# Performance work log

Measured on AMD Instinct MI355X. Metric: run time of the kernel, lower is better.

Reference implementation:

```python
import jax, jax.numpy as jnp
import numpy as np

N_NODES = 100000
N_EDGES = 1600000
IN_DIM, HID_DIM, OUT_DIM = 128, 128, 47
BN_EPS = 1e-5


def setup_inputs() -> dict:
    key = jax.random.key(0)
    ks = jax.random.split(key, 12)
    x = jax.random.normal(ks[0], (N_NODES, IN_DIM), dtype=jnp.float32)
    edge_index = jax.random.randint(ks[1], (2, N_EDGES), 0, N_NODES, dtype=jnp.int32)
    def glorot(k, fan_in, fan_out):
        s = jnp.sqrt(6.0 / (fan_in + fan_out))
        return jax.random.uniform(k, (fan_in, fan_out), jnp.float32, -s, s)
    return {
        "x": x,
        "edge_index": edge_index,
        "W0": glorot(ks[2], IN_DIM, HID_DIM), "b0": jnp.zeros((HID_DIM,), jnp.float32),
        "W1": glorot(ks[3], HID_DIM, HID_DIM), "b1": jnp.zeros((HID_DIM,), jnp.float32),
        "W2": glorot(ks[4], HID_DIM, OUT_DIM), "b2": jnp.zeros((OUT_DIM,), jnp.float32),
        "g0": jnp.ones((HID_DIM,), jnp.float32), "be0": jnp.zeros((HID_DIM,), jnp.float32),
        "g1": jnp.ones((HID_DIM,), jnp.float32), "be1": jnp.zeros((HID_DIM,), jnp.float32),
    }


def _gcn_norm(edge_index, n_nodes):
    # add self-loops, compute sym-normalized edge weights (PyG GCNConv default)
    loop = jnp.arange(n_nodes, dtype=edge_index.dtype)
    src = jnp.concatenate([edge_index[0], loop])
    dst = jnp.concatenate([edge_index[1], loop])
    deg = jax.ops.segment_sum(jnp.ones_like(dst, dtype=jnp.float32), dst,
                              num_segments=n_nodes)
    dinv = jnp.where(deg > 0, jax.lax.rsqrt(deg), 0.0)
    norm = dinv[src] * dinv[dst]  # [E + N]
    return src, dst, norm


def _conv(x, W, b, src, dst, norm, n_nodes):
    h = x @ W                                   # [N, d_out]
    msg = h[src] * norm[:, None]                # gather + scale
    out = jax.ops.segment_sum(msg, dst, num_segments=n_nodes)
    return out + b


def _batchnorm(h, gamma, beta):
    mean = jnp.mean(h, axis=0)
    var = jnp.mean(jnp.square(h - mean), axis=0)  # biased var (torch BN)
    return (h - mean) * jax.lax.rsqrt(var + BN_EPS) * gamma + beta


def reference(x, edge_index, W0, b0, W1, b1, W2, b2, g0, be0, g1, be1):
    n = x.shape[0]
    src, dst, norm = _gcn_norm(edge_index, n)
    h = _conv(x, W0, b0, src, dst, norm, n)
    h = jax.nn.relu(_batchnorm(h, g0, be0))     # dropout = identity (eval)
    h = _conv(h, W1, b1, src, dst, norm, n)
    h = jax.nn.relu(_batchnorm(h, g1, be1))
    h = _conv(h, W2, b2, src, dst, norm, n)
    return jax.nn.log_softmax(h, axis=-1)
```

## Files before the change

kernel.cpp:

```cpp
#include <hip/hip_runtime.h>
#include <math.h>

#define N_NODES 100000
#define N_EDGES 1600000
#define HID 128
#define OUTD 47
#define OSTR 48

#define NPB 128
#define NB 782
#define BCAP 2560
#define CHUNK 2048
#define NCHB 782
#define CWB 64

typedef short bf16x8 __attribute__((ext_vector_type(8)));
typedef float f32x4 __attribute__((ext_vector_type(4)));

__device__ inline unsigned short f2bf(float x) {
    union { float f; unsigned int u; } v; v.f = x;
    unsigned int r = v.u + 0x7fffu + ((v.u >> 16) & 1u);
    return (unsigned short)(r >> 16);
}
__device__ inline float bf_lo(unsigned int u) { return __uint_as_float(u << 16); }
__device__ inline float bf_hi(unsigned int u) { return __uint_as_float(u & 0xffff0000u); }

__device__ inline unsigned int src_chunk(unsigned int s) {
    return (s * 42950u) >> 28;
}


__global__ __launch_bounds__(256) void binA_k(
    const int* __restrict__ src, const int* __restrict__ dst,
    int* __restrict__ gcur, unsigned int* __restrict__ binned,
    const float* __restrict__ W0, const float* __restrict__ W1, const float* __restrict__ W2,
    unsigned short* __restrict__ Wt0, unsigned short* __restrict__ Wt1,
    unsigned short* __restrict__ Wt2)
{
    __shared__ unsigned int sortedL[CHUNK];
    __shared__ unsigned short bucketOf[CHUNK];
    __shared__ int cntL[NB];
    __shared__ int excL[NB];
    __shared__ int curL[NB];
    __shared__ int gposL[NB];
    __shared__ int partial[256];

    int t = threadIdx.x;

    if (blockIdx.x >= NCHB) {
        int i = (blockIdx.x - NCHB) * 256 + t;
        if (i < 16384) {
            int n = i >> 7, k = i & 127;
            Wt0[i] = f2bf(W0[k * 128 + n]);
            Wt1[i] = f2bf(W1[k * 128 + n]);
        }
        if (i < 48 * 128) {
            int n = i >> 7, k = i & 127;
            Wt2[i] = (n < OUTD) ? f2bf(W2[k * OUTD + n]) : (unsigned short)0;
        }
        return;
    }

    int e0 = blockIdx.x * CHUNK;

    for (int i = t; i < NB; i += 256) cntL[i] = 0;
    __syncthreads();

    for (int i = t; i < CHUNK; i += 256) {
        int e = e0 + i;
        if (e < N_EDGES) atomicAdd(&cntL[dst[e] >> 7], 1);
    }
    __syncthreads();

    int b4 = t * 4;
    int c0 = (b4 + 0 < NB) ? cntL[b4 + 0] : 0;
    int c1 = (b4 + 1 < NB) ? cntL[b4 + 1] : 0;
    int c2 = (b4 + 2 < NB) ? cntL[b4 + 2] : 0;
    int c3 = (b4 + 3 < NB) ? cntL[b4 + 3] : 0;
    int lsum = c0 + c1 + c2 + c3;
    partial[t] = lsum;
    __syncthreads();
    for (int off = 1; off < 256; off <<= 1) {
        int x = (t >= off) ? partial[t - off] : 0;
        __syncthreads();
        partial[t] += x;
        __syncthreads();
    }
    int pbase = partial[t] - lsum;
    if (b4 + 0 < NB) { excL[b4 + 0] = pbase;                curL[b4 + 0] = pbase; }
    if (b4 + 1 < NB) { excL[b4 + 1] = pbase + c0;           curL[b4 + 1] = pbase + c0; }
    if (b4 + 2 < NB) { excL[b4 + 2] = pbase + c0 + c1;      curL[b4 + 2] = pbase + c0 + c1; }
    if (b4 + 3 < NB) { excL[b4 + 3] = pbase + c0 + c1 + c2; curL[b4 + 3] = pbase + c0 + c1 + c2; }
    __syncthreads();

    int tot = partial[255];

    for (int i = t; i < CHUNK; i += 256) {
        int e = e0 + i;
        if (e < N_EDGES) {
            int d = dst[e];
            int s = src[e];
            int bkt = d >> 7;
            int pos = atomicAdd(&curL[bkt], 1);
            sortedL[pos] = ((unsigned int)s << 7) | (unsigned int)(d & 127);
            bucketOf[pos] = (unsigned short)bkt;
        }
    }
    __syncthreads();

    for (int b = t; b < NB; b += 256) {
        int c = cntL[b];
        gposL[b] = c ? atomicAdd(&gcur[b], c) : 0;
    }
    __syncthreads();

    for (int i = t; i < tot; i += 256) {
        unsigned int r = sortedL[i];
        int bkt = bucketOf[i];
        binned[(size_t)bkt * BCAP + gposL[bkt] + (i - excL[bkt])] = r;
    }
}


__global__ __launch_bounds__(256) void binB_k(
    const unsigned int* __restrict__ binned, const int* __restrict__ gcur,
    int2* __restrict__ rowse, float* __restrict__ dinv, int* __restrict__ colv)
{
    __shared__ unsigned int recL[BCAP];
    __shared__ int colL[BCAP];
    __shared__ int hist[2048];
    __shared__ int partial[256];

    int b = blockIdx.x, t = threadIdx.x;
    int cnt = gcur[b];
    int base = b * BCAP;
    const unsigned int* rp = binned + (size_t)b * BCAP;

    for (int i = t; i < 2048; i += 256) hist[i] = 0;
    __syncthreads();

    for (int i = t; i < cnt; i += 256) {
        unsigned int r = rp[i];
        recL[i] = r;
        unsigned int key = ((r & 127u) << 4) | src_chunk(r >> 7);
        atomicAdd(&hist[key], 1);
    }
    __syncthreads();

    int base8 = t * 8;
    int v[8], lsum = 0;
#pragma unroll
    for (int j = 0; j < 8; j++) { v[j] = hist[base8 + j]; lsum += v[j]; }
    partial[t] = lsum;
    __syncthreads();
    for (int off = 1; off < 256; off <<= 1) {
        int x = (t >= off) ? partial[t - off] : 0;
        __syncthreads();
        partial[t] += x;
        __syncthreads();
    }
    int run = partial[t] - lsum;
#pragma unroll
    for (int j = 0; j < 8; j++) { hist[base8 + j] = run; run += v[j]; }
    __syncthreads();

    if (t < NPB) {
        int node = b * NPB + t;
        if (node < N_NODES) {
            int start = hist[t << 4];
            int end = (t < NPB - 1) ? hist[(t + 1) << 4] : cnt;
            rowse[node] = make_int2(base + start, base + end);
            dinv[node] = rsqrtf((float)(end - start + 1));
        }
    }
    __syncthreads();

    for (int i = t; i < cnt; i += 256) {
        unsigned int r = recL[i];
        unsigned int key = ((r & 127u) << 4) | src_chunk(r >> 7);
        int pos = atomicAdd(&hist[key], 1);
        colL[pos] = (int)(r >> 7);
    }
    __syncthreads();
    for (int i = t; i < cnt; i += 256) colv[base + i] = colL[i];
}


template <int ABF16, int MODE, int NT, int OBF16>
__global__ __launch_bounds__(256) void gemm_k(
    const void* __restrict__ Ap, const unsigned short* __restrict__ Wt,
    const float* __restrict__ bnSum, const float* __restrict__ bnSq,
    const float* __restrict__ gam, const float* __restrict__ bet,
    const float* __restrict__ dinv, void* __restrict__ Outp,
    int ncols, int ostride)
{
    __shared__ unsigned short WtL[NT * 16][136];
    __shared__ float sS[128], sT[128];

    int t = threadIdx.x;
    if (MODE) {
        if (t < 128) {
            float mean = bnSum[t] * (1.0f / N_NODES);
            float var = bnSq[t] * (1.0f / N_NODES) - mean * mean;
            float inv = rsqrtf(var + 1e-5f);
            float s = gam[t] * inv;
            sS[t] = s;
            sT[t] = bet[t] - mean * s;
        }
    }

    const int TOT = NT * 16 * 128;
    for (int e = t * 8; e < TOT; e += 256 * 8) {
        int n = e >> 7, k = e & 127;
        uint4 v = *(const uint4*)(Wt + e);
        *(uint4*)&WtL[n][k] = v;
    }
    __syncthreads();

    int wave = t >> 6, lane = t & 63;
    int quad = lane >> 4, m16 = lane & 15;
    int rbase = blockIdx.x * 128 + wave * 32;

    f32x4 acc[2][NT];
#pragma unroll
    for (int rt = 0; rt < 2; rt++)
#pragma unroll
        for (int ct = 0; ct < NT; ct++) acc[rt][ct] = (f32x4){0.f, 0.f, 0.f, 0.f};

#pragma unroll
    for (int kc = 0; kc < 4; kc++) {
        int kb = kc * 32 + quad * 8;
        bf16x8 afrag[2];
#pragma unroll
        for (int rt = 0; rt < 2; rt++) {
            int row = rbase + rt * 16 + m16;
            bool rv = (row < N_NODES);
            if (ABF16) {
                uint4 v = make_uint4(0, 0, 0, 0);
                if (rv) v = *(const uint4*)((const unsigned short*)Ap + (size_t)row * 128 + kb);
                if (MODE) {
                    unsigned int uu[4] = {v.x, v.y, v.z, v.w};
                    unsigned short* fp = (unsigned short*)&afrag[rt];
#pragma unroll
                    for (int i = 0; i < 4; i++) {
                        int k0 = kb + 2 * i;
                        float lo = fmaxf(bf_lo(uu[i]) * sS[k0] + sT[k0], 0.f);
                        float hi = fmaxf(bf_hi(uu[i]) * sS[k0 + 1] + sT[k0 + 1], 0.f);
                        fp[2 * i] = f2bf(lo);
                        fp[2 * i + 1] = f2bf(hi);
                    }
                } else {
                    afrag[rt] = *(bf16x8*)&v;
                }
            } else {
                const float* ap = (const float*)Ap + (size_t)row * 128 + kb;
                float4 f0 = make_float4(0.f, 0.f, 0.f, 0.f), f1 = f0;
                if (rv) { f0 = *(const float4*)ap; f1 = *(const float4*)(ap + 4); }
                unsigned short* fp = (unsigned short*)&afrag[rt];
                fp[0] = f2bf(f0.x); fp[1] = f2bf(f0.y); fp[2] = f2bf(f0.z); fp[3] = f2bf(f0.w);
                fp[4] = f2bf(f1.x); fp[5] = f2bf(f1.y); fp[6] = f2bf(f1.z); fp[7] = f2bf(f1.w);
            }
        }
#pragma unroll
        for (int ct = 0; ct < NT; ct++) {
            bf16x8 bfrag = *(bf16x8*)&WtL[ct * 16 + m16][kb];
#pragma unroll
            for (int rt = 0; rt < 2; rt++)
                acc[rt][ct] = __builtin_amdgcn_mfma_f32_16x16x32_bf16(
                    afrag[rt], bfrag, acc[rt][ct], 0, 0, 0);
        }
    }

#pragma unroll
    for (int rt = 0; rt < 2; rt++)
#pragma unroll
        for (int r = 0; r < 4; r++) {
            int row = rbase + rt * 16 + quad * 4 + r;
            if (row < N_NODES) {
                float d = dinv[row];
#pragma unroll
                for (int ct = 0; ct < NT; ct++) {
                    int c = ct * 16 + m16;
                    if (c < ncols) {
                        float val = acc[rt][ct][r] * d;
                        if (OBF16)
                            ((unsigned short*)Outp)[(size_t)row * ostride + c] = f2bf(val);
                        else
                            ((float*)Outp)[(size_t)row * ostride + c] = val;
                    }
                }
            }
        }
}


__global__ __launch_bounds__(256) void agg_k(
    const unsigned int* __restrict__ H, const int2* __restrict__ rowse,
    const int* __restrict__ colv, const float* __restrict__ dinv,
    const float* __restrict__ bias, unsigned int* __restrict__ out)
{
    int gw = (blockIdx.x * 256 + threadIdx.x) >> 6;
    int lane = threadIdx.x & 63;
    if (gw >= N_NODES) return;
    int half = lane >> 5;
    int c = lane & 31;
    int2 se = rowse[gw];
    int rp = se.x, re = se.y;
    const uint2* H2 = (const uint2*)H;

    float a0 = 0.f, a1 = 0.f, a2 = 0.f, a3 = 0.f;
    if (half == 0) {
        uint2 u = H2[(size_t)gw * 32 + c];
        a0 = bf_lo(u.x); a1 = bf_hi(u.x); a2 = bf_lo(u.y); a3 = bf_hi(u.y);
    }

    for (int j0 = rp; j0 < re; j0 += 64) {
        int idx = (j0 + lane < re) ? colv[j0 + lane] : 0;
        int n = min(64, re - j0);
        int np = n >> 1;
        int t2 = 0;
        for (; t2 + 1 < np; t2 += 2) {
            int sa = __shfl(idx, 2 * t2 + half);
            int sb = __shfl(idx, 2 * t2 + 2 + half);
            uint2 ua = H2[(size_t)sa * 32 + c];
            uint2 ub = H2[(size_t)sb * 32 + c];
            a0 += bf_lo(ua.x) + bf_lo(ub.x);
            a1 += bf_hi(ua.x) + bf_hi(ub.x);
            a2 += bf_lo(ua.y) + bf_lo(ub.y);
            a3 += bf_hi(ua.y) + bf_hi(ub.y);
        }
        if (t2 < np) {
            int sa = __shfl(idx, 2 * t2 + half);
            uint2 ua = H2[(size_t)sa * 32 + c];
            a0 += bf_lo(ua.x); a1 += bf_hi(ua.x);
            a2 += bf_lo(ua.y); a3 += bf_hi(ua.y);
        }
        if (n & 1) {
            int sa = __shfl(idx, n - 1);
            if (half == 0) {
                uint2 ua = H2[(size_t)sa * 32 + c];
                a0 += bf_lo(ua.x); a1 += bf_hi(ua.x);
                a2 += bf_lo(ua.y); a3 += bf_hi(ua.y);
            }
        }
    }

    a0 += __shfl_xor(a0, 32);
    a1 += __shfl_xor(a1, 32);
    a2 += __shfl_xor(a2, 32);
    a3 += __shfl_xor(a3, 32);

    if (half == 0) {
        float d = dinv[gw];
        float4 b = ((const float4*)bias)[c];
        uint2 r;
        r.x = (unsigned int)f2bf(a0 * d + b.x) | ((unsigned int)f2bf(a1 * d + b.y) << 16);
        r.y = (unsigned int)f2bf(a2 * d + b.z) | ((unsigned int)f2bf(a3 * d + b.w) << 16);
        ((uint2*)out)[(size_t)gw * 32 + c] = r;
    }
}


__global__ __launch_bounds__(256) void agg_out_k(
    const unsigned int* __restrict__ H, const int2* __restrict__ rowse,
    const int* __restrict__ colv, const float* __restrict__ dinv,
    const float* __restrict__ b2, float* __restrict__ out)
{
    int gw = (blockIdx.x * 256 + threadIdx.x) >> 6;
    int lane = threadIdx.x & 63;
    if (gw >= N_NODES) return;
    int half = lane >> 5;
    int c = lane & 31;
    bool ld = c < 24;
    int2 se = rowse[gw];
    int rp = se.x, re = se.y;

    float ax = 0.f, ay = 0.f;
    if (half == 0 && ld) {
        unsigned int u = H[(size_t)gw * 24 + c];
        ax = bf_lo(u); ay = bf_hi(u);
    }

    for (int j0 = rp; j0 < re; j0 += 64) {
        int idx = (j0 + lane < re) ? colv[j0 + lane] : 0;
        int n = min(64, re - j0);
        int np = n >> 1;
        int t2 = 0;
        for (; t2 + 1 < np; t2 += 2) {
            int sa = __shfl(idx, 2 * t2 + half);
            int sb = __shfl(idx, 2 * t2 + 2 + half);
            if (ld) {
                unsigned int ua = H[(size_t)sa * 24 + c];
                unsigned int ub = H[(size_t)sb * 24 + c];
                ax += bf_lo(ua) + bf_lo(ub);
                ay += bf_hi(ua) + bf_hi(ub);
            }
        }
        if (t2 < np) {
            int sa = __shfl(idx, 2 * t2 + half);
            if (ld) {
                unsigned int ua = H[(size_t)sa * 24 + c];
                ax += bf_lo(ua); ay += bf_hi(ua);
            }
        }
        if (n & 1) {
            int sa = __shfl(idx, n - 1);
            if (half == 0 && ld) {
                unsigned int ua = H[(size_t)sa * 24 + c];
                ax += bf_lo(ua); ay += bf_hi(ua);
            }
        }
    }

    ax += __shfl_xor(ax, 32);
    ay += __shfl_xor(ay, 32);

    float d = dinv[gw];
    int c0 = c * 2, c1 = c * 2 + 1;
    float v0 = -INFINITY, v1 = -INFINITY;
    if (ld) {
        v0 = ax * d + b2[c0];
        if (c1 < OUTD) v1 = ay * d + b2[c1];
    }
    float m = fmaxf(v0, v1);
    for (int off = 16; off; off >>= 1) m = fmaxf(m, __shfl_xor(m, off));
    float e = 0.f;
    if (ld) {
        e = __expf(v0 - m);
        if (c1 < OUTD) e += __expf(v1 - m);
    }
    float sum = e;
    for (int off = 16; off; off >>= 1) sum += __shfl_xor(sum, off);
    float ls = logf(sum);
    if (half == 0 && ld) {
        out[(size_t)gw * OUTD + c0] = v0 - m - ls;
        if (c1 < OUTD) out[(size_t)gw * OUTD + c1] = v1 - m - ls;
    }
}


__global__ __launch_bounds__(256) void bnstats_k(const unsigned int* __restrict__ H,
                                                 float* __restrict__ sum,
                                                 float* __restrict__ sq)
{
    __shared__ float2 ls[256], lq[256];
    int t = threadIdx.x;
    int idx = blockIdx.x * 256 + t;
    int stride = gridDim.x * 256;
    float sx = 0.f, sy = 0.f, qx = 0.f, qy = 0.f;
    for (; idx < N_NODES * 64; idx += stride) {
        unsigned int u = H[idx];
        float x = bf_lo(u), y = bf_hi(u);
        sx += x; sy += y; qx += x * x; qy += y * y;
    }
    ls[t] = make_float2(sx, sy);
    lq[t] = make_float2(qx, qy);
    __syncthreads();
    if (t < 64) {
        float2 a = ls[t], b = ls[t + 64], c = ls[t + 128], d = ls[t + 192];
        float2 e = lq[t], f = lq[t + 64], g = lq[t + 128], h = lq[t + 192];
        int c0 = t * 2;
        atomicAdd(&sum[c0],     a.x + b.x + c.x + d.x);
        atomicAdd(&sum[c0 + 1], a.y + b.y + c.y + d.y);
        atomicAdd(&sq[c0],      e.x + f.x + g.x + h.x);
        atomicAdd(&sq[c0 + 1],  e.y + f.y + g.y + h.y);
    }
}


extern "C" void kernel_launch(void* const* d_in, const int* in_sizes, int n_in,
                              void* d_out, int out_size, void* d_ws, size_t ws_size,
                              hipStream_t stream)
{
    const float* x   = (const float*)d_in[0];
    const int*   ei  = (const int*)d_in[1];
    const float* W0  = (const float*)d_in[2];
    const float* b0  = (const float*)d_in[3];
    const float* W1  = (const float*)d_in[4];
    const float* b1  = (const float*)d_in[5];
    const float* W2  = (const float*)d_in[6];
    const float* b2  = (const float*)d_in[7];
    const float* g0  = (const float*)d_in[8];
    const float* be0 = (const float*)d_in[9];
    const float* g1  = (const float*)d_in[10];
    const float* be1 = (const float*)d_in[11];
    const int* srcv = ei;
    const int* dstv = ei + N_EDGES;

    char* w = (char*)d_ws;
    unsigned int* H0 = (unsigned int*)w;  w += (size_t)N_NODES * 128 * 2;
    unsigned int* H1 = (unsigned int*)w;  w += (size_t)N_NODES * 128 * 2;
    unsigned int* Hf = (unsigned int*)w;  w += (size_t)N_NODES * OSTR * 2;
    unsigned int* binned = (unsigned int*)w; w += (size_t)NB * BCAP * 4;
    int* colv = (int*)w;        w += (size_t)NB * BCAP * 4;
    unsigned short* Wt0 = (unsigned short*)w; w += 16384 * 2;
    unsigned short* Wt1 = (unsigned short*)w; w += 16384 * 2;
    unsigned short* Wt2 = (unsigned short*)w; w += 48 * 128 * 2;
    int2* rowse = (int2*)w;     w += (size_t)N_NODES * 8;
    float* dinv = (float*)w;    w += (size_t)N_NODES * 4;
    int* gcur = (int*)w;        w += 784 * 4;
    float* bnS0 = (float*)w;    w += 128 * 4;
    float* bnQ0 = (float*)w;    w += 128 * 4;
    float* bnS1 = (float*)w;    w += 128 * 4;
    float* bnQ1 = (float*)w;    w += 128 * 4;

    int gb = (N_NODES + 127) / 128;
    int ab = (N_NODES * 64 + 255) / 256;

    hipMemsetAsync(gcur, 0, (784 + 512) * 4, stream);

    binA_k<<<NCHB + CWB, 256, 0, stream>>>(srcv, dstv, gcur, binned,
                                           W0, W1, W2, Wt0, Wt1, Wt2);
    binB_k<<<NB, 256, 0, stream>>>(binned, gcur, rowse, dinv, colv);

    gemm_k<0, 0, 8, 1><<<gb, 256, 0, stream>>>(x, Wt0, nullptr, nullptr, nullptr, nullptr,
                                               dinv, H0, 128, 128);
    agg_k<<<ab, 256, 0, stream>>>(H0, rowse, colv, dinv, b0, H1);
    bnstats_k<<<512, 256, 0, stream>>>(H1, bnS0, bnQ0);

    gemm_k<1, 1, 8, 1><<<gb, 256, 0, stream>>>(H1, Wt1, bnS0, bnQ0, g0, be0,
                                               dinv, H0, 128, 128);
    agg_k<<<ab, 256, 0, stream>>>(H0, rowse, colv, dinv, b1, H1);
    bnstats_k<<<512, 256, 0, stream>>>(H1, bnS1, bnQ1);

    gemm_k<1, 1, 3, 1><<<gb, 256, 0, stream>>>(H1, Wt2, bnS1, bnQ1, g1, be1,
                                               dinv, Hf, OUTD, OSTR);
    agg_out_k<<<ab, 256, 0, stream>>>(Hf, rowse, colv, dinv, b2, (float*)d_out);
}
```

Before: 483.5 us.

## Store features in column-tiled layout and aggregate per 16-column tile

Feature matrices are now stored as 16-column bf16 tiles laid out tile-major ([tile][node][16]). The aggregation kernels give each tile its own block, so one 8-lane group handles one node's 32-byte slice. The intent is to shrink each gather's working set so it stays resident in cache and to raise reuse of scattered neighbor rows. Log-softmax moves into a separate kernel, and bnstats reduces per tile. This adds launches, extra passes over the output and narrower 32-byte gathers per edge.

After: 645.7 us. +33.5%, slower.

```diff
diff --git a/kernel.cpp b/kernel.cpp
--- a/kernel.cpp
+++ b/kernel.cpp
@@ -5,7 +5,6 @@
 #define N_EDGES 1600000
 #define HID 128
 #define OUTD 47
-#define OSTR 48
 
 #define NPB 128
 #define NB 782
@@ -186,13 +185,13 @@
 }
 
 
-template <int ABF16, int MODE, int NT, int OBF16>
+template <int ABF16, int MODE, int NT>
 __global__ __launch_bounds__(256) void gemm_k(
     const void* __restrict__ Ap, const unsigned short* __restrict__ Wt,
     const float* __restrict__ bnSum, const float* __restrict__ bnSq,
     const float* __restrict__ gam, const float* __restrict__ bet,
-    const float* __restrict__ dinv, void* __restrict__ Outp,
-    int ncols, int ostride)
+    const float* __restrict__ dinv, unsigned short* __restrict__ Outp,
+    int ncols)
 {
     __shared__ unsigned short WtL[NT * 16][136];
     __shared__ float sS[128], sT[128];
@@ -237,7 +236,11 @@
             bool rv = (row < N_NODES);
             if (ABF16) {
                 uint4 v = make_uint4(0, 0, 0, 0);
-                if (rv) v = *(const uint4*)((const unsigned short*)Ap + (size_t)row * 128 + kb);
+                if (rv) {
+                    const unsigned int* hp = (const unsigned int*)Ap
+                        + ((size_t)(kb >> 4) * N_NODES + row) * 8 + ((kb & 8) ? 4 : 0);
+                    v = *(const uint4*)hp;
+                }
                 if (MODE) {
                     unsigned int uu[4] = {v.x, v.y, v.z, v.w};
                     unsigned short* fp = (unsigned short*)&afrag[rt];
@@ -283,10 +286,7 @@
                     int c = ct * 16 + m16;
                     if (c < ncols) {
                         float val = acc[rt][ct][r] * d;
-                        if (OBF16)
-                            ((unsigned short*)Outp)[(size_t)row * ostride + c] = f2bf(val);
-                        else
-                            ((float*)Outp)[(size_t)row * ostride + c] = val;
+                        Outp[((size_t)ct * N_NODES + row) * 16 + m16] = f2bf(val);
                     }
                 }
             }
@@ -299,65 +299,43 @@
     const int* __restrict__ colv, const float* __restrict__ dinv,
     const float* __restrict__ bias, unsigned int* __restrict__ out)
 {
-    int gw = (blockIdx.x * 256 + threadIdx.x) >> 6;
+    int T = blockIdx.x & 7;
     int lane = threadIdx.x & 63;
-    if (gw >= N_NODES) return;
-    int half = lane >> 5;
-    int c = lane & 31;
-    int2 se = rowse[gw];
-    int rp = se.x, re = se.y;
-    const uint2* H2 = (const uint2*)H;
-
-    float a0 = 0.f, a1 = 0.f, a2 = 0.f, a3 = 0.f;
-    if (half == 0) {
-        uint2 u = H2[(size_t)gw * 32 + c];
-        a0 = bf_lo(u.x); a1 = bf_hi(u.x); a2 = bf_lo(u.y); a3 = bf_hi(u.y);
-    }
-
-    for (int j0 = rp; j0 < re; j0 += 64) {
-        int idx = (j0 + lane < re) ? colv[j0 + lane] : 0;
-        int n = min(64, re - j0);
-        int np = n >> 1;
-        int t2 = 0;
-        for (; t2 + 1 < np; t2 += 2) {
-            int sa = __shfl(idx, 2 * t2 + half);
-            int sb = __shfl(idx, 2 * t2 + 2 + half);
-            uint2 ua = H2[(size_t)sa * 32 + c];
-            uint2 ub = H2[(size_t)sb * 32 + c];
-            a0 += bf_lo(ua.x) + bf_lo(ub.x);
-            a1 += bf_hi(ua.x) + bf_hi(ub.x);
-            a2 += bf_lo(ua.y) + bf_lo(ub.y);
-            a3 += bf_hi(ua.y) + bf_hi(ub.y);
-        }
-        if (t2 < np) {
-            int sa = __shfl(idx, 2 * t2 + half);
-            uint2 ua = H2[(size_t)sa * 32 + c];
-            a0 += bf_lo(ua.x); a1 += bf_hi(ua.x);
-            a2 += bf_lo(ua.y); a3 += bf_hi(ua.y);
-        }
-        if (n & 1) {
-            int sa = __shfl(idx, n - 1);
-            if (half == 0) {
-                uint2 ua = H2[(size_t)sa * 32 + c];
-                a0 += bf_lo(ua.x); a1 += bf_hi(ua.x);
-                a2 += bf_lo(ua.y); a3 += bf_hi(ua.y);
-            }
-        }
-    }
-
-    a0 += __shfl_xor(a0, 32);
-    a1 += __shfl_xor(a1, 32);
-    a2 += __shfl_xor(a2, 32);
-    a3 += __shfl_xor(a3, 32);
-
-    if (half == 0) {
-        float d = dinv[gw];
-        float4 b = ((const float4*)bias)[c];
-        uint2 r;
-        r.x = (unsigned int)f2bf(a0 * d + b.x) | ((unsigned int)f2bf(a1 * d + b.y) << 16);
-        r.y = (unsigned int)f2bf(a2 * d + b.z) | ((unsigned int)f2bf(a3 * d + b.w) << 16);
-        ((uint2*)out)[(size_t)gw * 32 + c] = r;
-    }
+    int oct = lane >> 3, e = lane & 7;
+    int node = (blockIdx.x >> 3) * 32 + (threadIdx.x >> 6) * 8 + oct;
+    const unsigned int* Hs = H + (size_t)T * (N_NODES * 8);
+
+    int2 se = rowse[node];
+    int rp = se.x, d = se.y - se.x;
+
+    unsigned int u = Hs[(size_t)node * 8 + e];
+    float a0 = bf_lo(u), a1 = bf_hi(u);
+
+    int j = 0;
+    for (; j + 3 < d; j += 4) {
+        int s0 = __builtin_nontemporal_load(colv + rp + j);
+        int s1 = __builtin_nontemporal_load(colv + rp + j + 1);
+        int s2 = __builtin_nontemporal_load(colv + rp + j + 2);
+        int s3 = __builtin_nontemporal_load(colv + rp + j + 3);
+        unsigned int u0 = Hs[(size_t)s0 * 8 + e];
+        unsigned int u1 = Hs[(size_t)s1 * 8 + e];
+        unsigned int u2 = Hs[(size_t)s2 * 8 + e];
+        unsigned int u3 = Hs[(size_t)s3 * 8 + e];
+        a0 += bf_lo(u0) + bf_lo(u1) + bf_lo(u2) + bf_lo(u3);
+        a1 += bf_hi(u0) + bf_hi(u1) + bf_hi(u2) + bf_hi(u3);
+    }
+    for (; j < d; j++) {
+        int s0 = __builtin_nontemporal_load(colv + rp + j);
+        unsigned int u0 = Hs[(size_t)s0 * 8 + e];
+        a0 += bf_lo(u0);
+        a1 += bf_hi(u0);
+    }
+
+    float dv = dinv[node];
+    float2 b = ((const float2*)bias)[T * 8 + e];
+    unsigned int r = (unsigned int)f2bf(a0 * dv + b.x)
+                   | ((unsigned int)f2bf(a1 * dv + b.y) << 16);
+    out[(size_t)T * (N_NODES * 8) + (size_t)node * 8 + e] = r;
 }
 
 
@@ -366,76 +344,67 @@
     const int* __restrict__ colv, const float* __restrict__ dinv,
     const float* __restrict__ b2, float* __restrict__ out)
 {
-    int gw = (blockIdx.x * 256 + threadIdx.x) >> 6;
+    int q = blockIdx.x & 7;
+    if (q >= 6) return;
+    int T = q % 3, half = q / 3;
+    int g = blockIdx.x >> 3;
+    if (half == 1 && g >= 1562) return;
     int lane = threadIdx.x & 63;
-    if (gw >= N_NODES) return;
-    int half = lane >> 5;
-    int c = lane & 31;
-    bool ld = c < 24;
-    int2 se = rowse[gw];
-    int rp = se.x, re = se.y;
-
-    float ax = 0.f, ay = 0.f;
-    if (half == 0 && ld) {
-        unsigned int u = H[(size_t)gw * 24 + c];
-        ax = bf_lo(u); ay = bf_hi(u);
-    }
-
-    for (int j0 = rp; j0 < re; j0 += 64) {
-        int idx = (j0 + lane < re) ? colv[j0 + lane] : 0;
-        int n = min(64, re - j0);
-        int np = n >> 1;
-        int t2 = 0;
-        for (; t2 + 1 < np; t2 += 2) {
-            int sa = __shfl(idx, 2 * t2 + half);
-            int sb = __shfl(idx, 2 * t2 + 2 + half);
-            if (ld) {
-                unsigned int ua = H[(size_t)sa * 24 + c];
-                unsigned int ub = H[(size_t)sb * 24 + c];
-                ax += bf_lo(ua) + bf_lo(ub);
-                ay += bf_hi(ua) + bf_hi(ub);
-            }
-        }
-        if (t2 < np) {
-            int sa = __shfl(idx, 2 * t2 + half);
-            if (ld) {
-                unsigned int ua = H[(size_t)sa * 24 + c];
-                ax += bf_lo(ua); ay += bf_hi(ua);
-            }
-        }
-        if (n & 1) {
-            int sa = __shfl(idx, n - 1);
-            if (half == 0 && ld) {
-                unsigned int ua = H[(size_t)sa * 24 + c];
-                ax += bf_lo(ua); ay += bf_hi(ua);
-            }
-        }
-    }
-
-    ax += __shfl_xor(ax, 32);
-    ay += __shfl_xor(ay, 32);
-
-    float d = dinv[gw];
-    int c0 = c * 2, c1 = c * 2 + 1;
-    float v0 = -INFINITY, v1 = -INFINITY;
-    if (ld) {
-        v0 = ax * d + b2[c0];
-        if (c1 < OUTD) v1 = ay * d + b2[c1];
-    }
+    int oct = lane >> 3, e = lane & 7;
+    int node = half * 50016 + g * 32 + (threadIdx.x >> 6) * 8 + oct;
+    const unsigned int* Hs = H + (size_t)T * (N_NODES * 8);
+
+    int2 se = rowse[node];
+    int rp = se.x, d = se.y - se.x;
+
+    unsigned int u = Hs[(size_t)node * 8 + e];
+    float a0 = bf_lo(u), a1 = bf_hi(u);
+
+    int j = 0;
+    for (; j + 3 < d; j += 4) {
+        int s0 = __builtin_nontemporal_load(colv + rp + j);
+        int s1 = __builtin_nontemporal_load(colv + rp + j + 1);
+        int s2 = __builtin_nontemporal_load(colv + rp + j + 2);
+        int s3 = __builtin_nontemporal_load(colv + rp + j + 3);
+        unsigned int u0 = Hs[(size_t)s0 * 8 + e];
+        unsigned int u1 = Hs[(size_t)s1 * 8 + e];
+        unsigned int u2 = Hs[(size_t)s2 * 8 + e];
+        unsigned int u3 = Hs[(size_t)s3 * 8 + e];
+        a0 += bf_lo(u0) + bf_lo(u1) + bf_lo(u2) + bf_lo(u3);
+        a1 += bf_hi(u0) + bf_hi(u1) + bf_hi(u2) + bf_hi(u3);
+    }
+    for (; j < d; j++) {
+        int s0 = __builtin_nontemporal_load(colv + rp + j);
+        unsigned int u0 = Hs[(size_t)s0 * 8 + e];
+        a0 += bf_lo(u0);
+        a1 += bf_hi(u0);
+    }
+
+    float dv = dinv[node];
+    int ch = 16 * T + 2 * e;
+    float* op = out + (size_t)node * OUTD;
+    op[ch] = a0 * dv + b2[ch];
+    if (ch + 1 < OUTD) op[ch + 1] = a1 * dv + b2[ch + 1];
+}
+
+
+__global__ __launch_bounds__(256) void lsm_k(float* __restrict__ out)
+{
+    int lane = threadIdx.x & 63;
+    int sub = lane >> 5, cp = lane & 31;
+    int node = (blockIdx.x * 4 + (threadIdx.x >> 6)) * 2 + sub;
+    int ch = cp * 2;
+    float* op = out + (size_t)node * OUTD;
+    float v0 = (ch < OUTD) ? op[ch] : -INFINITY;
+    float v1 = (ch + 1 < OUTD) ? op[ch + 1] : -INFINITY;
     float m = fmaxf(v0, v1);
-    for (int off = 16; off; off >>= 1) m = fmaxf(m, __shfl_xor(m, off));
-    float e = 0.f;
-    if (ld) {
-        e = __expf(v0 - m);
-        if (c1 < OUTD) e += __expf(v1 - m);
-    }
-    float sum = e;
-    for (int off = 16; off; off >>= 1) sum += __shfl_xor(sum, off);
-    float ls = logf(sum);
-    if (half == 0 && ld) {
-        out[(size_t)gw * OUTD + c0] = v0 - m - ls;
-        if (c1 < OUTD) out[(size_t)gw * OUTD + c1] = v1 - m - ls;
-    }
+    for (int off = 1; off < 32; off <<= 1) m = fmaxf(m, __shfl_xor(m, off));
+    float s = ((ch < OUTD) ? __expf(v0 - m) : 0.f)
+            + ((ch + 1 < OUTD) ? __expf(v1 - m) : 0.f);
+    for (int off = 1; off < 32; off <<= 1) s += __shfl_xor(s, off);
+    float ls = m + logf(s);
+    if (ch < OUTD) op[ch] = v0 - ls;
+    if (ch + 1 < OUTD) op[ch + 1] = v1 - ls;
 }
 
 
@@ -445,25 +414,30 @@
 {
     __shared__ float2 ls[256], lq[256];
     int t = threadIdx.x;
-    int idx = blockIdx.x * 256 + t;
-    int stride = gridDim.x * 256;
+    int tile = blockIdx.x & 7;
+    const unsigned int* Hp = H + (size_t)tile * (N_NODES * 8);
     float sx = 0.f, sy = 0.f, qx = 0.f, qy = 0.f;
-    for (; idx < N_NODES * 64; idx += stride) {
-        unsigned int u = H[idx];
+    for (int i = (blockIdx.x >> 3) * 256 + t; i < N_NODES * 8; i += 64 * 256) {
+        unsigned int u = Hp[i];
         float x = bf_lo(u), y = bf_hi(u);
         sx += x; sy += y; qx += x * x; qy += y * y;
     }
     ls[t] = make_float2(sx, sy);
     lq[t] = make_float2(qx, qy);
     __syncthreads();
-    if (t < 64) {
-        float2 a = ls[t], b = ls[t + 64], c = ls[t + 128], d = ls[t + 192];
-        float2 e = lq[t], f = lq[t + 64], g = lq[t + 128], h = lq[t + 192];
-        int c0 = t * 2;
-        atomicAdd(&sum[c0],     a.x + b.x + c.x + d.x);
-        atomicAdd(&sum[c0 + 1], a.y + b.y + c.y + d.y);
-        atomicAdd(&sq[c0],      e.x + f.x + g.x + h.x);
-        atomicAdd(&sq[c0 + 1],  e.y + f.y + g.y + h.y);
+    for (int off = 128; off >= 8; off >>= 1) {
+        if (t < off) {
+            ls[t].x += ls[t + off].x; ls[t].y += ls[t + off].y;
+            lq[t].x += lq[t + off].x; lq[t].y += lq[t + off].y;
+        }
+        __syncthreads();
+    }
+    if (t < 8) {
+        int c0 = tile * 16 + 2 * t;
+        atomicAdd(&sum[c0],     ls[t].x);
+        atomicAdd(&sum[c0 + 1], ls[t].y);
+        atomicAdd(&sq[c0],      lq[t].x);
+        atomicAdd(&sq[c0 + 1],  lq[t].y);
     }
 }
 
@@ -490,7 +464,7 @@
     char* w = (char*)d_ws;
     unsigned int* H0 = (unsigned int*)w;  w += (size_t)N_NODES * 128 * 2;
     unsigned int* H1 = (unsigned int*)w;  w += (size_t)N_NODES * 128 * 2;
-    unsigned int* Hf = (unsigned int*)w;  w += (size_t)N_NODES * OSTR * 2;
+    unsigned int* Hf = (unsigned int*)w;  w += (size_t)N_NODES * 48 * 2;
     unsigned int* binned = (unsigned int*)w; w += (size_t)NB * BCAP * 4;
     int* colv = (int*)w;        w += (size_t)NB * BCAP * 4;
     unsigned short* Wt0 = (unsigned short*)w; w += 16384 * 2;
@@ -505,7 +479,9 @@
     float* bnQ1 = (float*)w;    w += 128 * 4;
 
     int gb = (N_NODES + 127) / 128;
-    int ab = (N_NODES * 64 + 255) / 256;
+    int agb = 3125 * 8;
+    int aob = 1563 * 8;
+    int lsb = 12500;
 
     hipMemsetAsync(gcur, 0, (784 + 512) * 4, stream);
 
@@ -513,17 +489,18 @@
                                            W0, W1, W2, Wt0, Wt1, Wt2);
     binB_k<<<NB, 256, 0, stream>>>(binned, gcur, rowse, dinv, colv);
 
-    gemm_k<0, 0, 8, 1><<<gb, 256, 0, stream>>>(x, Wt0, nullptr, nullptr, nullptr, nullptr,
-                                               dinv, H0, 128, 128);
-    agg_k<<<ab, 256, 0, stream>>>(H0, rowse, colv, dinv, b0, H1);
+    gemm_k<0, 0, 8><<<gb, 256, 0, stream>>>(x, Wt0, nullptr, nullptr, nullptr, nullptr,
+                                            dinv, (unsigned short*)H0, 128);
+    agg_k<<<agb, 256, 0, stream>>>(H0, rowse, colv, dinv, b0, H1);
     bnstats_k<<<512, 256, 0, stream>>>(H1, bnS0, bnQ0);
 
-    gemm_k<1, 1, 8, 1><<<gb, 256, 0, stream>>>(H1, Wt1, bnS0, bnQ0, g0, be0,
-                                               dinv, H0, 128, 128);
-    agg_k<<<ab, 256, 0, stream>>>(H0, rowse, colv, dinv, b1, H1);
+    gemm_k<1, 1, 8><<<gb, 256, 0, stream>>>(H1, Wt1, bnS0, bnQ0, g0, be0,
+                                            dinv, (unsigned short*)H0, 128);
+    agg_k<<<agb, 256, 0, stream>>>(H0, rowse, colv, dinv, b1, H1);
     bnstats_k<<<512, 256, 0, stream>>>(H1, bnS1, bnQ1);
 
-    gemm_k<1, 1, 3, 1><<<gb, 256, 0, stream>>>(H1, Wt2, bnS1, bnQ1, g1, be1,
-                                               dinv, Hf, OUTD, OSTR);
-    agg_out_k<<<ab, 256, 0, stream>>>(Hf, rowse, colv, dinv, b2, (float*)d_out);
-}
+    gemm_k<1, 1, 3><<<gb, 256, 0, stream>>>(H1, Wt2, bnS1, bnQ1, g1, be1,
+                                            dinv, (unsigned short*)Hf, 48);
+    agg_out_k<<<aob, 256, 0, stream>>>(Hf, rowse, colv, dinv, b2, (float*)d_out);
+    lsm_k<<<lsb, 256, 0, stream>>>((float*)d_out);
+}
```
